# Optimization experiments

Measured on AMD Instinct MI355X. Metric: run time of the kernel, lower is better.

## Reference

```python
import jax, jax.numpy as jnp
import numpy as np

B, T, D, H, OUT = 1024, 2048, 5, 64, 128


def _lstm_layer(x, Wih, Whh, bih, bhh):
    """PyTorch-convention LSTM layer. x: [B,T,Din]; gate order i,f,g,o."""
    b, t = x.shape[0], x.shape[1]
    h = Whh.shape[1]
    # Precompute input projections for all timesteps (the only big GEMM).
    xp = jnp.einsum('btd,gd->btg', x, Wih) + bih + bhh        # [B,T,4H]
    xp = jnp.swapaxes(xp, 0, 1)                               # [T,B,4H]

    def step(carry, xt):
        hprev, cprev = carry
        gates = xt + hprev @ Whh.T                            # [B,4H]
        i, f, g, o = jnp.split(gates, 4, axis=-1)
        i = jax.nn.sigmoid(i)
        f = jax.nn.sigmoid(f)
        g = jnp.tanh(g)
        o = jax.nn.sigmoid(o)
        c = f * cprev + i * g
        hnew = o * jnp.tanh(c)
        return (hnew, c), hnew

    h0 = jnp.zeros((b, h), x.dtype)
    (hT, cT), hs = jax.lax.scan(step, (h0, h0), xp)
    return jnp.swapaxes(hs, 0, 1), hT                         # [B,T,H], [B,H]


def setup_inputs() -> dict:
    key = jax.random.key(0)
    ks = jax.random.split(key, 11)
    s = 1.0 / np.sqrt(H)  # PyTorch LSTM init range

    def u(k, shape):
        return jax.random.uniform(k, shape, jnp.float32, -s, s)

    return {
        'x': jax.random.normal(ks[0], (B, T, D), jnp.float32),
        'W_ih0': u(ks[1], (4 * H, D)),
        'W_hh0': u(ks[2], (4 * H, H)),
        'b_ih0': u(ks[3], (4 * H,)),
        'b_hh0': u(ks[4], (4 * H,)),
        'W_ih1': u(ks[5], (4 * H, H)),
        'W_hh1': u(ks[6], (4 * H, H)),
        'b_ih1': u(ks[7], (4 * H,)),
        'b_hh1': u(ks[8], (4 * H,)),
        'W_fc': u(ks[9], (OUT, H)),
        'b_fc': u(ks[10], (OUT,)),
    }


def reference(x, W_ih0, W_hh0, b_ih0, b_hh0, W_ih1, W_hh1, b_ih1, b_hh1, W_fc, b_fc):
    # Layer 1 over raw 5-dim signal; inter-layer dropout is inactive at inference.
    y1, _ = _lstm_layer(x, W_ih0, W_hh0, b_ih0, b_hh0)
    # Layer 2; only its final hidden state hn[-1] is used downstream.
    _, h2 = _lstm_layer(y1, W_ih1, W_hh1, b_ih1, b_hh1)
    return jax.nn.relu(h2 @ W_fc.T + b_fc)                    # [B,128]
```

## Files before the change

kernel.cpp:

```cpp
#include <hip/hip_runtime.h>
#include <math.h>

#define BATCH 1024
#define TSEQ  2048
#define DIN   5
#define H     64
#define BT    4
#define SSTR  144
#define NOUT  128

typedef _Float16 f16x8 __attribute__((ext_vector_type(8)));
typedef float    f32x4 __attribute__((ext_vector_type(4)));

#if __has_builtin(__builtin_amdgcn_rcpf)
__device__ __forceinline__ float rcp_fast(float x) { return __builtin_amdgcn_rcpf(x); }
#else
__device__ __forceinline__ float rcp_fast(float x) { return 1.0f / x; }
#endif

#define LOG2E 1.44269504088896f

__device__ __forceinline__ float sigm2(float s) {
    return rcp_fast(1.0f + __builtin_amdgcn_exp2f(-s));
}
__device__ __forceinline__ float tanh2(float s) {
    return fmaf(-2.0f, rcp_fast(__builtin_amdgcn_exp2f(s) + 1.0f), 1.0f);
}

__global__ __launch_bounds__(512)
void lstm_mfma(const float* __restrict__ x,
               const float* __restrict__ Wih0, const float* __restrict__ Whh0,
               const float* __restrict__ bih0, const float* __restrict__ bhh0,
               const float* __restrict__ Wih1, const float* __restrict__ Whh1,
               const float* __restrict__ bih1, const float* __restrict__ bhh1,
               const float* __restrict__ Wfc,  const float* __restrict__ bfc,
               float* __restrict__ out)
{
    __shared__ alignas(16) _Float16 S[2][BT * SSTR];
    __shared__ alignas(16) float    h2f[BT][H];

    const int tid  = threadIdx.x;
    const int w    = tid >> 6;
    const int lane = tid & 63;
    const int col  = lane & 15;
    const int q    = lane >> 4;
    const int ww   = w & 3;
    const int lay  = w >> 2;
    const int hu   = 16 * ww + col;
    const int b0   = blockIdx.x * BT;

    for (int j = tid; j < 2 * BT * SSTR; j += 512)
        ((_Float16*)S)[j] = (_Float16)0.0f;

    const float sgl[4] = {LOG2E, LOG2E, 2.0f * LOG2E, LOG2E};

    f16x8 Bf[4][4];
    f32x4 bC[4];
    #pragma unroll
    for (int g = 0; g < 4; ++g) {
        const int   row = g * 64 + hu;
        const float sg  = sgl[g];
        const float* Wa = lay ? (Wih1 + row * H) : (Whh0 + row * H);
        f16x8 f0, f1, f2, f3;
        #pragma unroll
        for (int j = 0; j < 8; ++j) {
            f0[j] = (_Float16)(Wa[q * 8 + j] * sg);
            f1[j] = (_Float16)(Wa[32 + q * 8 + j] * sg);
        }
        if (lay) {
            const float* Wb = Whh1 + row * H;
            #pragma unroll
            for (int j = 0; j < 8; ++j) {
                f2[j] = (_Float16)(Wb[q * 8 + j] * sg);
                f3[j] = (_Float16)(Wb[32 + q * 8 + j] * sg);
            }
        } else {
            #pragma unroll
            for (int j = 0; j < 8; ++j) {
                const int kk = q * 8 + j;
                f2[j] = (_Float16)(kk < DIN ? Wih0[row * DIN + kk] * sg : 0.0f);
                f3[j] = (_Float16)0.0f;
            }
        }
        Bf[g][0] = f0; Bf[g][1] = f1; Bf[g][2] = f2; Bf[g][3] = f3;
        const float bb = (lay ? (bih1[row] + bhh1[row])
                              : (bih0[row] + bhh0[row])) * sg;
        bC[g] = f32x4{bb, bb, bb, bb};
    }

    const float* xp = x + (size_t)(b0 + (col >> 2)) * TSEQ * DIN;
    f16x8 ax = {(_Float16)0.0f, (_Float16)0.0f, (_Float16)0.0f, (_Float16)0.0f,
                (_Float16)0.0f, (_Float16)0.0f, (_Float16)0.0f, (_Float16)0.0f};
    f32x4 dx[4];
    if (lay == 0) {
        if (q == 0) {
            ax[0] = (_Float16)xp[0]; ax[1] = (_Float16)xp[1];
            ax[2] = (_Float16)xp[2]; ax[3] = (_Float16)xp[3];
            ax[4] = (_Float16)xp[4];
        }
        #pragma unroll
        for (int g = 0; g < 4; ++g)
            dx[g] = __builtin_amdgcn_mfma_f32_16x16x32_f16(ax, Bf[g][2], bC[g], 0, 0, 0);
        xp += DIN;
    }

    const int ab  = (col >> 2) * SSTR + q * 8;
    const int wb1 = q * SSTR + hu;
    const int wb2 = q * SSTR + 64 + hu;
    float cst = 0.0f, h2fin = 0.0f;

    __syncthreads();

    #pragma unroll 1
    for (int i = 0; i <= TSEQ; ++i) {
        const _Float16* rb = S[(i + 1) & 1];
        _Float16*       wbuf = S[i & 1];

        if (lay == 0) {
            const bool xld = (q == 0) && (i + 1 < TSEQ);
            float x0, x1, x2, x3, x4;
            if (xld) { x0 = xp[0]; x1 = xp[1]; x2 = xp[2]; x3 = xp[3]; x4 = xp[4]; }

            f16x8 a0 = *(const f16x8*)&rb[ab];
            f16x8 a1 = *(const f16x8*)&rb[ab + 32];
            f32x4 d[4];
            #pragma unroll
            for (int g = 0; g < 4; ++g) {
                d[g] = __builtin_amdgcn_mfma_f32_16x16x32_f16(a0, Bf[g][0], dx[g], 0, 0, 0);
                d[g] = __builtin_amdgcn_mfma_f32_16x16x32_f16(a1, Bf[g][1], d[g], 0, 0, 0);
            }
            if (i < TSEQ) {
                float iv = sigm2(d[0][0]);
                float fv = sigm2(d[1][0]);
                float gv = tanh2(d[2][0]);
                float ov = sigm2(d[3][0]);
                cst = fmaf(fv, cst, iv * gv);
                wbuf[wb1] = (_Float16)(ov * tanh2(2.0f * LOG2E * cst));
            }
            if (xld) {
                ax[0] = (_Float16)x0; ax[1] = (_Float16)x1;
                ax[2] = (_Float16)x2; ax[3] = (_Float16)x3;
                ax[4] = (_Float16)x4;
            }
            #pragma unroll
            for (int g = 0; g < 4; ++g)
                dx[g] = __builtin_amdgcn_mfma_f32_16x16x32_f16(ax, Bf[g][2], bC[g], 0, 0, 0);
            xp += DIN;
        } else {
            f16x8 ay0 = *(const f16x8*)&rb[ab];
            f16x8 ay1 = *(const f16x8*)&rb[ab + 32];
            f16x8 ah0 = *(const f16x8*)&rb[ab + 64];
            f16x8 ah1 = *(const f16x8*)&rb[ab + 96];
            f32x4 d[4];
            #pragma unroll
            for (int g = 0; g < 4; ++g) {
                d[g] = __builtin_amdgcn_mfma_f32_16x16x32_f16(ay0, Bf[g][0], bC[g], 0, 0, 0);
                d[g] = __builtin_amdgcn_mfma_f32_16x16x32_f16(ay1, Bf[g][1], d[g], 0, 0, 0);
                d[g] = __builtin_amdgcn_mfma_f32_16x16x32_f16(ah0, Bf[g][2], d[g], 0, 0, 0);
                d[g] = __builtin_amdgcn_mfma_f32_16x16x32_f16(ah1, Bf[g][3], d[g], 0, 0, 0);
            }
            if (i > 0) {
                float iv = sigm2(d[0][0]);
                float fv = sigm2(d[1][0]);
                float gv = tanh2(d[2][0]);
                float ov = sigm2(d[3][0]);
                cst = fmaf(fv, cst, iv * gv);
                h2fin = ov * tanh2(2.0f * LOG2E * cst);
                wbuf[wb2] = (_Float16)h2fin;
            }
        }
        __syncthreads();
    }

    if (lay) h2f[q][hu] = h2fin;
    __syncthreads();
    {
        const int e = tid >> 7;
        const int o = tid & (NOUT - 1);
        const float4* wr = (const float4*)(Wfc + o * H);
        const float*  hv = h2f[e];
        float s0 = 0.f, s1 = 0.f, s2 = 0.f, s3 = 0.f;
        #pragma unroll
        for (int k = 0; k < H / 4; ++k) {
            float4 wv = wr[k];
            s0 = fmaf(wv.x, hv[4 * k + 0], s0);
            s1 = fmaf(wv.y, hv[4 * k + 1], s1);
            s2 = fmaf(wv.z, hv[4 * k + 2], s2);
            s3 = fmaf(wv.w, hv[4 * k + 3], s3);
        }
        float acc = bfc[o] + (s0 + s1) + (s2 + s3);
        out[(size_t)(b0 + e) * NOUT + o] = fmaxf(acc, 0.0f);
    }
}

extern "C" void kernel_launch(void* const* d_in, const int* in_sizes, int n_in,
                              void* d_out, int out_size, void* d_ws, size_t ws_size,
                              hipStream_t stream) {
    const float* x    = (const float*)d_in[0];
    const float* Wih0 = (const float*)d_in[1];
    const float* Whh0 = (const float*)d_in[2];
    const float* bih0 = (const float*)d_in[3];
    const float* bhh0 = (const float*)d_in[4];
    const float* Wih1 = (const float*)d_in[5];
    const float* Whh1 = (const float*)d_in[6];
    const float* bih1 = (const float*)d_in[7];
    const float* bhh1 = (const float*)d_in[8];
    const float* Wfc  = (const float*)d_in[9];
    const float* bfc  = (const float*)d_in[10];
    float* out = (float*)d_out;

    lstm_mfma<<<dim3(BATCH / BT), dim3(512), 0, stream>>>(
        x, Wih0, Whh0, bih0, bhh0, Wih1, Whh1, bih1, bhh1, Wfc, bfc, out);
}
```

Before: 988.6 us.

## Replace per-step block barrier with flag-based producer/consumer ring between LSTM layers

Replaces the lockstep __syncthreads per timestep with LDS ring buffers of depth DEP and per-wave progress flags, so layer-1 waves can run ahead of layer-2 waves and each waits only on the flags it depends on. Layer 2 starts its recurrent MFMAs before waiting for the layer-1 output of the current step, hiding part of the latency. The cost is spin-polling on volatile LDS flags, extra fences, and reliance on LDS memory ordering being correct without a full barrier.

After: 1.375 ms. 39.1% more time.

```diff
diff --git a/kernel.cpp b/kernel.cpp
--- a/kernel.cpp
+++ b/kernel.cpp
@@ -6,7 +6,8 @@
 #define DIN   5
 #define H     64
 #define BT    4
-#define SSTR  144
+#define DEP   4
+#define RSTR  80
 #define NOUT  128
 
 typedef _Float16 f16x8 __attribute__((ext_vector_type(8)));
@@ -27,8 +28,21 @@
     return fmaf(-2.0f, rcp_fast(__builtin_amdgcn_exp2f(s) + 1.0f), 1.0f);
 }
 
+__device__ __forceinline__ int imin(int a, int b) { return a < b ? a : b; }
+
+__device__ __forceinline__ int wait_min_ge(const int* p, int tgt) {
+    volatile const int* v = p;
+    int m;
+    do {
+        int a = v[0], b = v[1], c = v[2], d = v[3];
+        m = imin(imin(a, b), imin(c, d));
+    } while (m < tgt);
+    __threadfence_block();
+    return m;
+}
+
 __global__ __launch_bounds__(512)
-void lstm_mfma(const float* __restrict__ x,
+void lstm_pipe(const float* __restrict__ x,
                const float* __restrict__ Wih0, const float* __restrict__ Whh0,
                const float* __restrict__ bih0, const float* __restrict__ bhh0,
                const float* __restrict__ Wih1, const float* __restrict__ Whh1,
@@ -36,8 +50,10 @@
                const float* __restrict__ Wfc,  const float* __restrict__ bfc,
                float* __restrict__ out)
 {
-    __shared__ alignas(16) _Float16 S[2][BT * SSTR];
+    __shared__ alignas(16) _Float16 ring1[DEP][BT * RSTR];
+    __shared__ alignas(16) _Float16 ring2[DEP][BT * RSTR];
     __shared__ alignas(16) float    h2f[BT][H];
+    __shared__ alignas(16) int      flg[8];
 
     const int tid  = threadIdx.x;
     const int w    = tid >> 6;
@@ -49,8 +65,11 @@
     const int hu   = 16 * ww + col;
     const int b0   = blockIdx.x * BT;
 
-    for (int j = tid; j < 2 * BT * SSTR; j += 512)
-        ((_Float16*)S)[j] = (_Float16)0.0f;
+    for (int j = tid; j < DEP * BT * RSTR; j += 512) {
+        ((_Float16*)ring1)[j] = (_Float16)0.0f;
+        ((_Float16*)ring2)[j] = (_Float16)0.0f;
+    }
+    if (tid < 8) flg[tid] = 0;
 
     const float sgl[4] = {LOG2E, LOG2E, 2.0f * LOG2E, LOG2E};
 
@@ -88,11 +107,16 @@
         bC[g] = f32x4{bb, bb, bb, bb};
     }
 
-    const float* xp = x + (size_t)(b0 + (col >> 2)) * TSEQ * DIN;
-    f16x8 ax = {(_Float16)0.0f, (_Float16)0.0f, (_Float16)0.0f, (_Float16)0.0f,
-                (_Float16)0.0f, (_Float16)0.0f, (_Float16)0.0f, (_Float16)0.0f};
-    f32x4 dx[4];
+    const int ab    = (col >> 2) * RSTR + q * 8;
+    const int wslot = q * RSTR + hu;
+
+    __syncthreads();
+
     if (lay == 0) {
+        const float* xp = x + (size_t)(b0 + (col >> 2)) * TSEQ * DIN;
+        f16x8 ax = {(_Float16)0.0f, (_Float16)0.0f, (_Float16)0.0f, (_Float16)0.0f,
+                    (_Float16)0.0f, (_Float16)0.0f, (_Float16)0.0f, (_Float16)0.0f};
+        f32x4 dx[4];
         if (q == 0) {
             ax[0] = (_Float16)xp[0]; ax[1] = (_Float16)xp[1];
             ax[2] = (_Float16)xp[2]; ax[3] = (_Float16)xp[3];
@@ -102,25 +126,18 @@
         for (int g = 0; g < 4; ++g)
             dx[g] = __builtin_amdgcn_mfma_f32_16x16x32_f16(ax, Bf[g][2], bC[g], 0, 0, 0);
         xp += DIN;
-    }
-
-    const int ab  = (col >> 2) * SSTR + q * 8;
-    const int wb1 = q * SSTR + hu;
-    const int wb2 = q * SSTR + 64 + hu;
-    float cst = 0.0f, h2fin = 0.0f;
-
-    __syncthreads();
-
-    #pragma unroll 1
-    for (int i = 0; i <= TSEQ; ++i) {
-        const _Float16* rb = S[(i + 1) & 1];
-        _Float16*       wbuf = S[i & 1];
-
-        if (lay == 0) {
-            const bool xld = (q == 0) && (i + 1 < TSEQ);
+
+        float cst = 0.0f;
+        int s1 = 0, s2 = 0;
+        #pragma unroll 1
+        for (int t = 0; t < TSEQ; ++t) {
+            if (s1 < t) s1 = wait_min_ge(flg, t);
+
+            const bool xld = (q == 0) && (t + 1 < TSEQ);
             float x0, x1, x2, x3, x4;
             if (xld) { x0 = xp[0]; x1 = xp[1]; x2 = xp[2]; x3 = xp[3]; x4 = xp[4]; }
 
+            const _Float16* rb = ring1[(t + DEP - 1) & (DEP - 1)];
             f16x8 a0 = *(const f16x8*)&rb[ab];
             f16x8 a1 = *(const f16x8*)&rb[ab + 32];
             f32x4 d[4];
@@ -129,14 +146,18 @@
                 d[g] = __builtin_amdgcn_mfma_f32_16x16x32_f16(a0, Bf[g][0], dx[g], 0, 0, 0);
                 d[g] = __builtin_amdgcn_mfma_f32_16x16x32_f16(a1, Bf[g][1], d[g], 0, 0, 0);
             }
-            if (i < TSEQ) {
-                float iv = sigm2(d[0][0]);
-                float fv = sigm2(d[1][0]);
-                float gv = tanh2(d[2][0]);
-                float ov = sigm2(d[3][0]);
-                cst = fmaf(fv, cst, iv * gv);
-                wbuf[wb1] = (_Float16)(ov * tanh2(2.0f * LOG2E * cst));
-            }
+
+            if (t >= DEP && s2 < t - DEP + 1) s2 = wait_min_ge(flg + 4, t - DEP + 1);
+
+            float iv = sigm2(d[0][0]);
+            float fv = sigm2(d[1][0]);
+            float gv = tanh2(d[2][0]);
+            float ov = sigm2(d[3][0]);
+            cst = fmaf(fv, cst, iv * gv);
+            ring1[t & (DEP - 1)][wslot] = (_Float16)(ov * tanh2(2.0f * LOG2E * cst));
+            __threadfence_block();
+            if (lane == 0) ((volatile int*)flg)[ww] = t + 1;
+
             if (xld) {
                 ax[0] = (_Float16)x0; ax[1] = (_Float16)x1;
                 ax[2] = (_Float16)x2; ax[3] = (_Float16)x3;
@@ -146,34 +167,49 @@
             for (int g = 0; g < 4; ++g)
                 dx[g] = __builtin_amdgcn_mfma_f32_16x16x32_f16(ax, Bf[g][2], bC[g], 0, 0, 0);
             xp += DIN;
-        } else {
-            f16x8 ay0 = *(const f16x8*)&rb[ab];
-            f16x8 ay1 = *(const f16x8*)&rb[ab + 32];
-            f16x8 ah0 = *(const f16x8*)&rb[ab + 64];
-            f16x8 ah1 = *(const f16x8*)&rb[ab + 96];
+        }
+    } else {
+        float cst = 0.0f, h2fin = 0.0f;
+        int m1 = 0, m2 = 0;
+        #pragma unroll 1
+        for (int t = 0; t < TSEQ; ++t) {
+            if (m2 < t) m2 = wait_min_ge(flg + 4, t);
+
+            const _Float16* rh = ring2[(t + DEP - 1) & (DEP - 1)];
+            f16x8 ah0 = *(const f16x8*)&rh[ab];
+            f16x8 ah1 = *(const f16x8*)&rh[ab + 32];
             f32x4 d[4];
             #pragma unroll
             for (int g = 0; g < 4; ++g) {
-                d[g] = __builtin_amdgcn_mfma_f32_16x16x32_f16(ay0, Bf[g][0], bC[g], 0, 0, 0);
+                d[g] = __builtin_amdgcn_mfma_f32_16x16x32_f16(ah0, Bf[g][2], bC[g], 0, 0, 0);
+                d[g] = __builtin_amdgcn_mfma_f32_16x16x32_f16(ah1, Bf[g][3], d[g], 0, 0, 0);
+            }
+
+            if (m1 < t + 1) m1 = wait_min_ge(flg, t + 1);
+            const _Float16* ry = ring1[t & (DEP - 1)];
+            f16x8 ay0 = *(const f16x8*)&ry[ab];
+            f16x8 ay1 = *(const f16x8*)&ry[ab + 32];
+            #pragma unroll
+            for (int g = 0; g < 4; ++g) {
+                d[g] = __builtin_amdgcn_mfma_f32_16x16x32_f16(ay0, Bf[g][0], d[g], 0, 0, 0);
                 d[g] = __builtin_amdgcn_mfma_f32_16x16x32_f16(ay1, Bf[g][1], d[g], 0, 0, 0);
-                d[g] = __builtin_amdgcn_mfma_f32_16x16x32_f16(ah0, Bf[g][2], d[g], 0, 0, 0);
-                d[g] = __builtin_amdgcn_mfma_f32_16x16x32_f16(ah1, Bf[g][3], d[g], 0, 0, 0);
-            }
-            if (i > 0) {
-                float iv = sigm2(d[0][0]);
-                float fv = sigm2(d[1][0]);
-                float gv = tanh2(d[2][0]);
-                float ov = sigm2(d[3][0]);
-                cst = fmaf(fv, cst, iv * gv);
-                h2fin = ov * tanh2(2.0f * LOG2E * cst);
-                wbuf[wb2] = (_Float16)h2fin;
-            }
-        }
-        __syncthreads();
-    }
-
-    if (lay) h2f[q][hu] = h2fin;
+            }
+
+            float iv = sigm2(d[0][0]);
+            float fv = sigm2(d[1][0]);
+            float gv = tanh2(d[2][0]);
+            float ov = sigm2(d[3][0]);
+            cst = fmaf(fv, cst, iv * gv);
+            h2fin = ov * tanh2(2.0f * LOG2E * cst);
+            ring2[t & (DEP - 1)][wslot] = (_Float16)h2fin;
+            __threadfence_block();
+            if (lane == 0) ((volatile int*)flg)[4 + ww] = t + 1;
+        }
+        h2f[q][hu] = h2fin;
+    }
+
     __syncthreads();
+
     {
         const int e = tid >> 7;
         const int o = tid & (NOUT - 1);
@@ -209,6 +245,6 @@
     const float* bfc  = (const float*)d_in[10];
     float* out = (float*)d_out;
 
-    lstm_mfma<<<dim3(BATCH / BT), dim3(512), 0, stream>>>(
+    lstm_pipe<<<dim3(BATCH / BT), dim3(512), 0, stream>>>(
         x, Wih0, Whh0, bih0, bhh0, Wih1, Whh1, bih1, bhh1, Wfc, bfc, out);
 }
```
